# Optimization experiments

Measured on AMD Instinct MI355X. Metric: run time of the kernel, lower is better.

## Reference

```python
import jax, jax.numpy as jnp
import numpy as np

N_NODES = 100000
N_EDGES = 1600000
D_IN, D_HID, D_OUT = 64, 64, 32


def _glorot(key, shape):
    fan_in, fan_out = shape[0], shape[1]
    lim = np.sqrt(6.0 / (fan_in + fan_out)).astype(np.float32)
    return jax.random.uniform(key, shape, jnp.float32, -lim, lim)


def setup_inputs() -> dict:
    key = jax.random.key(0)
    ks = jax.random.split(key, 12)
    x = jax.random.normal(ks[0], (N_NODES, D_IN), jnp.float32)
    edge_index = jax.random.randint(ks[1], (2, N_EDGES), 0, N_NODES, jnp.int64)
    return {
        "x": x,
        "edge_index": edge_index,
        # SAGEConv 1 (in->hid): lin_l (aggregated neighbors, with bias), lin_r (root, no bias)
        "Wl1": _glorot(ks[2], (D_IN, D_HID)),
        "Wr1": _glorot(ks[3], (D_IN, D_HID)),
        "b1": jnp.zeros((D_HID,), jnp.float32),
        # SAGEConv 2 (hid->out)
        "Wl2": _glorot(ks[4], (D_HID, D_OUT)),
        "Wr2": _glorot(ks[5], (D_HID, D_OUT)),
        "b2": jnp.zeros((D_OUT,), jnp.float32),
        # trust head: Linear(32,16) -> ReLU -> Linear(16,1) -> Sigmoid (dropout inert in eval)
        "Wt1": _glorot(ks[6], (D_OUT, 16)),
        "bt1": jnp.zeros((16,), jnp.float32),
        "Wt2": _glorot(ks[7], (16, 1)),
        "bt2": jnp.zeros((1,), jnp.float32),
    }


def _sage_conv(x, src, dst, Wl, Wr, b):
    # mean-aggregate neighbor messages: msg flows src -> dst
    msg = x[src]                                              # [E, d] gather
    agg_sum = jax.ops.segment_sum(msg, dst, num_segments=N_NODES)
    deg = jax.ops.segment_sum(jnp.ones((src.shape[0],), x.dtype), dst,
                              num_segments=N_NODES)
    agg = agg_sum / jnp.maximum(deg, 1.0)[:, None]            # zero-degree -> 0
    return agg @ Wl + x @ Wr + b


def reference(x, edge_index, Wl1, Wr1, b1, Wl2, Wr2, b2, Wt1, bt1, Wt2, bt2):
    src, dst = edge_index[0], edge_index[1]
    h = _sage_conv(x, src, dst, Wl1, Wr1, b1)
    h = jax.nn.relu(h)                    # dropout p=0.3 inert in eval
    h = _sage_conv(h, src, dst, Wl2, Wr2, b2)
    t = jax.nn.relu(h @ Wt1 + bt1)        # dropout p=0.2 inert in eval
    trust = jax.nn.sigmoid(t @ Wt2 + bt2)
    return h, trust
```

## Files before the change

kernel.cpp:

```cpp
#include <hip/hip_runtime.h>
#include <math.h>


#define NBUCK   1563
#define BCAP    1536
#define BKCHUNK 4096

typedef __attribute__((ext_vector_type(8))) __bf16 bf16x8;
typedef __attribute__((ext_vector_type(4))) float  f32x4;

union BU { bf16x8 v; unsigned short u[8]; };

__device__ inline unsigned short f2bf(float x) {
    unsigned u = __float_as_uint(x);
    unsigned r = u + 0x7fffu + ((u >> 16) & 1u);
    return (unsigned short)(r >> 16);
}
__device__ inline unsigned pack2(float a, float b) {
    return (unsigned)f2bf(a) | ((unsigned)f2bf(b) << 16);
}
__device__ inline float bflo(unsigned u) { return __uint_as_float(u << 16); }
__device__ inline float bfhi(unsigned u) { return __uint_as_float(u & 0xffff0000u); }
__device__ inline float bf2f(unsigned short h) { return __uint_as_float((unsigned)h << 16); }

__global__ __launch_bounds__(256) void k_w(
    const float* __restrict__ Wl1, const float* __restrict__ Wr1,
    unsigned short* __restrict__ Wf)
{
    int tid = threadIdx.x;
    for (int idx = tid; idx < 1024; idx += 256) {
        int q = idx >> 6;
        int l = idx & 63;
        int pass = q >> 3, nf = (q >> 1) & 3, kf = q & 1;
        const float* W = pass ? Wr1 : Wl1;
        int col  = nf * 16 + (l & 15);
        int krow = kf * 32 + (l >> 4) * 8;
        unsigned short hi8[8], lo8[8];
        #pragma unroll
        for (int e = 0; e < 8; ++e) {
            float w = W[(krow + e) * 64 + col];
            unsigned short h = f2bf(w);
            hi8[e] = h;
            lo8[e] = f2bf(w - bf2f(h));
        }
        #pragma unroll
        for (int e = 0; e < 8; ++e) {
            Wf[(q * 2 + 0) * 512 + l * 8 + e] = hi8[e];
            Wf[(q * 2 + 1) * 512 + l * 8 + e] = lo8[e];
        }
    }
}

__global__ __launch_bounds__(256) void k_m1(
    const float* __restrict__ x,
    const unsigned short* __restrict__ Wf, const float* __restrict__ b1,
    unsigned* __restrict__ u16b, float* __restrict__ v,
    const int* __restrict__ src, const int* __restrict__ dst,
    int* __restrict__ gcnt, unsigned* __restrict__ pairs,
    int N, int E, int GB, int BKB)
{
    __shared__ int hist[NBUCK];
    int tid = threadIdx.x;
    int g = blockIdx.x / 5, r5 = blockIdx.x % 5;

    if (r5 == 4) {
        if (g >= BKB) return;
        int e0 = g * BKCHUNK;
        int e1 = min(e0 + BKCHUNK, E);

        for (int i = tid; i < NBUCK; i += 256) hist[i] = 0;
        __syncthreads();
        for (int e = e0 + tid; e < e1; e += 256)
            atomicAdd(&hist[((unsigned)dst[e]) >> 6], 1);
        __syncthreads();
        int cnt[7], base[7];
        #pragma unroll
        for (int t = 0; t < 7; ++t) {
            int i = tid + t * 256;
            cnt[t] = (i < NBUCK) ? hist[i] : 0;
        }
        #pragma unroll
        for (int t = 0; t < 7; ++t) {
            int i = tid + t * 256;
            base[t] = (i < NBUCK) ? atomicAdd(&gcnt[i], cnt[t]) : 0;
        }
        #pragma unroll
        for (int t = 0; t < 7; ++t) {
            int i = tid + t * 256;
            if (i < NBUCK) hist[i] = i * BCAP + base[t];
        }
        __syncthreads();
        for (int e = e0 + tid; e < e1; e += 256) {
            int t = dst[e];
            int b = ((unsigned)t) >> 6;
            int pos = atomicAdd(&hist[b], 1);
            if (pos < (b + 1) * BCAP)
                pairs[pos] = (unsigned)src[e] | ((unsigned)(t & 63) << 17);
        }
        return;
    }

    int tile = 4 * g + r5;
    if (tile >= GB) return;
    int nblk = tile * 64;

    int l  = tid & 63, wv = tid >> 6;
    int la = l & 15,   g4 = l >> 4;
    int arow = nblk + wv * 16 + la;
    bool rowOK = (arow < N);

    BU ahi[2], alo[2];
    #pragma unroll
    for (int kf = 0; kf < 2; ++kf) {
        float xv[8];
        if (rowOK) {
            const float* xp = &x[(size_t)arow * 64 + kf * 32 + g4 * 8];
            float4 p0 = *(const float4*)xp;
            float4 p1 = *(const float4*)(xp + 4);
            xv[0] = p0.x; xv[1] = p0.y; xv[2] = p0.z; xv[3] = p0.w;
            xv[4] = p1.x; xv[5] = p1.y; xv[6] = p1.z; xv[7] = p1.w;
        } else {
            #pragma unroll
            for (int e = 0; e < 8; ++e) xv[e] = 0.0f;
        }
        #pragma unroll
        for (int e = 0; e < 8; ++e) {
            unsigned short h = f2bf(xv[e]);
            ahi[kf].u[e] = h;
            alo[kf].u[e] = f2bf(xv[e] - bf2f(h));
        }
    }

    unsigned short* u16 = (unsigned short*)u16b;

    #pragma unroll
    for (int pass = 0; pass < 2; ++pass) {
        #pragma unroll
        for (int nf = 0; nf < 4; ++nf) {
            int n0 = nf * 16;
            f32x4 acc = {0.f, 0.f, 0.f, 0.f};
            #pragma unroll
            for (int kf = 0; kf < 2; ++kf) {
                int q2 = ((pass * 4 + nf) * 2 + kf) * 2;
                bf16x8 bhi = *(const bf16x8*)&Wf[(q2 + 0) * 512 + l * 8];
                bf16x8 blo = *(const bf16x8*)&Wf[(q2 + 1) * 512 + l * 8];
                acc = __builtin_amdgcn_mfma_f32_16x16x32_bf16(ahi[kf].v, bhi, acc, 0, 0, 0);
                acc = __builtin_amdgcn_mfma_f32_16x16x32_bf16(alo[kf].v, bhi, acc, 0, 0, 0);
                acc = __builtin_amdgcn_mfma_f32_16x16x32_bf16(ahi[kf].v, blo, acc, 0, 0, 0);
            }
            if (pass == 0) {
                #pragma unroll
                for (int r = 0; r < 4; ++r) {
                    int nd = nblk + wv * 16 + g4 * 4 + r;
                    if (nd < N)
                        u16[(size_t)nd * 64 + n0 + la] = f2bf(acc[r]);
                }
            } else {
                float bb = b1[n0 + la];
                #pragma unroll
                for (int r = 0; r < 4; ++r) {
                    int nd = nblk + wv * 16 + g4 * 4 + r;
                    if (nd < N)
                        v[(size_t)nd * 64 + n0 + la] = acc[r] + bb;
                }
            }
        }
    }
}

__global__ __launch_bounds__(512) void k_m2(
    const unsigned* __restrict__ pairs, const int* __restrict__ gcnt,
    const unsigned* __restrict__ u16b, const float* __restrict__ v,
    const float* __restrict__ Wl2, const float* __restrict__ Wr2,
    const float* __restrict__ b2,
    unsigned* __restrict__ P16b, float* __restrict__ Qout,
    int2* __restrict__ nodeOff, int* __restrict__ adjG, int N)
{
    __shared__ float sH[64 * 66];
    __shared__ float sW[64 * 64];
    __shared__ int   sAdj[BCAP];
    __shared__ int   sOff[65];
    __shared__ int   sCur[64];
    int tid = threadIdx.x;
    int b = blockIdx.x;
    int nodeBase = b * 64;
    int base = b * BCAP;
    int count = min(gcnt[b], BCAP);
    const unsigned* pp = pairs + (size_t)b * BCAP;

    for (int i = tid * 4; i < 64 * 64; i += 2048) {
        int k = i >> 6, n = i & 63;
        const float* Wsrc = (n < 32) ? (Wl2 + k * 32 + n) : (Wr2 + k * 32 + (n - 32));
        *(float4*)&sW[k * 64 + n] = *(const float4*)Wsrc;
    }
    if (tid < 64) sCur[tid] = 0;
    __syncthreads();

    for (int j = tid; j < count; j += 512)
        atomicAdd(&sCur[(pp[j] >> 17) & 63], 1);
    __syncthreads();
    if (tid < 64) {
        int c = sCur[tid];
        int incl = c;
        #pragma unroll
        for (int off = 1; off < 64; off <<= 1) {
            int t = __shfl_up(incl, off);
            if (tid >= off) incl += t;
        }
        sOff[tid] = incl - c;
        if (tid == 63) sOff[64] = incl;
    }
    __syncthreads();
    if (tid < 64) {
        sCur[tid] = sOff[tid];
        int node = nodeBase + tid;
        if (node < N)
            nodeOff[node] = make_int2(base + sOff[tid], sOff[tid + 1] - sOff[tid]);
    }
    __syncthreads();
    for (int j = tid; j < count; j += 512) {
        unsigned e = pp[j];
        int pos = atomicAdd(&sCur[(e >> 17) & 63], 1);
        sAdj[pos] = (int)(e & 0x1FFFFu);
    }
    __syncthreads();
    for (int j = tid; j < count; j += 512) adjG[base + j] = sAdj[j];

    int hw = tid >> 5, lane = tid & 31;
    for (int r = 0; r < 4; ++r) {
        int nl = hw * 4 + r;
        int node = nodeBase + nl;
        float h0 = 0.0f, h1v = 0.0f;
        if (node < N) {
            int beg = sOff[nl], end = sOff[nl + 1];
            float lo[8] = {0,0,0,0,0,0,0,0}, hi[8] = {0,0,0,0,0,0,0,0};
            int i = beg;
            for (; i + 8 <= end; i += 8) {
                int s[8];
                #pragma unroll
                for (int j = 0; j < 8; ++j) s[j] = sAdj[i + j];
                #pragma unroll
                for (int j = 0; j < 8; ++j) {
                    unsigned w = u16b[(size_t)s[j] * 32 + lane];
                    lo[j] += bflo(w); hi[j] += bfhi(w);
                }
            }
            for (; i < end; ++i) {
                unsigned w = u16b[(size_t)sAdj[i] * 32 + lane];
                lo[0] += bflo(w); hi[0] += bfhi(w);
            }
            float mlo = ((lo[0]+lo[1])+(lo[2]+lo[3])) + ((lo[4]+lo[5])+(lo[6]+lo[7]));
            float mhi = ((hi[0]+hi[1])+(hi[2]+hi[3])) + ((hi[4]+hi[5])+(hi[6]+hi[7]));
            int deg = end - beg;
            float invd = (deg > 0) ? 1.0f / (float)deg : 1.0f;
            float2 vv = ((const float2*)v)[(size_t)node * 32 + lane];
            h0  = fmaxf(mlo * invd + vv.x, 0.0f);
            h1v = fmaxf(mhi * invd + vv.y, 0.0f);
        }
        *(float2*)&sH[nl * 66 + 2 * lane] = make_float2(h0, h1v);
    }
    __syncthreads();

    int ng = tid & 15;
    int mg = tid >> 4;
    int m0 = mg * 2, n0 = ng * 4;

    float acc[2][4];
    #pragma unroll
    for (int mi = 0; mi < 2; ++mi)
        #pragma unroll
        for (int ni = 0; ni < 4; ++ni) acc[mi][ni] = 0.0f;

    #pragma unroll 8
    for (int k = 0; k < 64; ++k) {
        float a0 = sH[(m0 + 0) * 66 + k];
        float a1 = sH[(m0 + 1) * 66 + k];
        float4 w = *(float4*)&sW[k * 64 + n0];
        float wv[4] = {w.x, w.y, w.z, w.w};
        #pragma unroll
        for (int ni = 0; ni < 4; ++ni) {
            acc[0][ni] = fmaf(a0, wv[ni], acc[0][ni]);
            acc[1][ni] = fmaf(a1, wv[ni], acc[1][ni]);
        }
    }

    if (n0 < 32) {
        #pragma unroll
        for (int mi = 0; mi < 2; ++mi) {
            int node = nodeBase + m0 + mi;
            if (node >= N) continue;
            uint2 pk;
            pk.x = pack2(acc[mi][0], acc[mi][1]);
            pk.y = pack2(acc[mi][2], acc[mi][3]);
            *(uint2*)&P16b[(size_t)node * 16 + (n0 >> 1)] = pk;
        }
    } else {
        float4 b0 = *(const float4*)&b2[n0 - 32];
        #pragma unroll
        for (int mi = 0; mi < 2; ++mi) {
            int node = nodeBase + m0 + mi;
            if (node >= N) continue;
            *(float4*)&Qout[(size_t)node * 32 + (n0 - 32)] =
                make_float4(acc[mi][0]+b0.x, acc[mi][1]+b0.y,
                            acc[mi][2]+b0.z, acc[mi][3]+b0.w);
        }
    }
}

__global__ __launch_bounds__(256) void k_a2(
    const int2* __restrict__ nodeOff, const int* __restrict__ adj,
    const unsigned* __restrict__ P16b, const float* __restrict__ Q,
    const float* __restrict__ Wt1, const float* __restrict__ bt1,
    const float* __restrict__ Wt2, const float* __restrict__ bt2,
    float* __restrict__ out_h, float* __restrict__ out_trust, int N)
{
    __shared__ float sWt1[32 * 16];
    __shared__ float sWt2[16];
    for (int i = threadIdx.x; i < 512; i += 256) sWt1[i] = Wt1[i];
    if (threadIdx.x < 16) sWt2[threadIdx.x] = Wt2[threadIdx.x];
    __syncthreads();

    int n = blockIdx.x * 16 + (threadIdx.x >> 4);
    int lane = threadIdx.x & 15;
    if (n >= N) return;

    int2 od = nodeOff[n];
    int beg = od.x, end = od.x + od.y;
    float lo[8] = {0,0,0,0,0,0,0,0}, hi[8] = {0,0,0,0,0,0,0,0};
    int i = beg;
    for (; i + 8 <= end; i += 8) {
        int s[8];
        #pragma unroll
        for (int j = 0; j < 8; ++j) s[j] = adj[i + j];
        #pragma unroll
        for (int j = 0; j < 8; ++j) {
            unsigned w = P16b[(size_t)s[j] * 16 + lane];
            lo[j] += bflo(w); hi[j] += bfhi(w);
        }
    }
    for (; i < end; ++i) {
        unsigned w = P16b[(size_t)adj[i] * 16 + lane];
        lo[0] += bflo(w); hi[0] += bfhi(w);
    }
    float invd = (od.y > 0) ? 1.0f / (float)od.y : 1.0f;
    float mlo = (((lo[0]+lo[1])+(lo[2]+lo[3])) + ((lo[4]+lo[5])+(lo[6]+lo[7]))) * invd;
    float mhi = (((hi[0]+hi[1])+(hi[2]+hi[3])) + ((hi[4]+hi[5])+(hi[6]+hi[7]))) * invd;

    float2 qv = ((const float2*)Q)[(size_t)n * 16 + lane];
    float hx = mlo + qv.x;
    float hy = mhi + qv.y;

    ((float2*)out_h)[(size_t)n * 16 + lane] = make_float2(hx, hy);

    float t = bt1[lane];
    #pragma unroll
    for (int k = 0; k < 16; ++k) {
        float hlo = __shfl(hx, k, 16);
        float hhi = __shfl(hy, k, 16);
        t += hlo * sWt1[(2 * k) * 16 + lane] + hhi * sWt1[(2 * k + 1) * 16 + lane];
    }
    t = fmaxf(t, 0.0f);
    float z = t * sWt2[lane];
    z += __shfl_xor(z, 1);
    z += __shfl_xor(z, 2);
    z += __shfl_xor(z, 4);
    z += __shfl_xor(z, 8);
    if (lane == 0) out_trust[n] = 1.0f / (1.0f + expf(-(z + bt2[0])));
}


extern "C" void kernel_launch(void* const* d_in, const int* in_sizes, int n_in,
                              void* d_out, int out_size, void* d_ws, size_t ws_size,
                              hipStream_t stream)
{
    const float* x   = (const float*)d_in[0];
    const int*   ei  = (const int*)d_in[1];
    const float* Wl1 = (const float*)d_in[2];
    const float* Wr1 = (const float*)d_in[3];
    const float* b1  = (const float*)d_in[4];
    const float* Wl2 = (const float*)d_in[5];
    const float* Wr2 = (const float*)d_in[6];
    const float* b2  = (const float*)d_in[7];
    const float* Wt1 = (const float*)d_in[8];
    const float* bt1 = (const float*)d_in[9];
    const float* Wt2 = (const float*)d_in[10];
    const float* bt2 = (const float*)d_in[11];

    const int N = in_sizes[0] / 64;
    const int E = in_sizes[1] / 2;
    const int* src = ei;
    const int* dst = ei + E;

    unsigned* pairs  = (unsigned*)d_ws;
    unsigned* u16b   = pairs + (size_t)NBUCK * BCAP;
    float*    v      = (float*)(u16b + (size_t)N * 32);
    unsigned* P16b   = (unsigned*)(v + (size_t)N * 64);
    float*    Q      = (float*)(P16b + (size_t)N * 16);
    int2*     nodeOff= (int2*)(Q + (size_t)N * 32);
    int*      adj    = (int*)(nodeOff + N);
    int*      gcnt   = adj + (size_t)NBUCK * BCAP;
    unsigned short* Wf = (unsigned short*)(gcnt + 2048);

    hipMemsetAsync(gcnt, 0, 2048 * sizeof(int), stream);

    k_w<<<1, 256, 0, stream>>>(Wl1, Wr1, Wf);

    const int GB  = (N + 63) / 64;
    const int BKB = (E + BKCHUNK - 1) / BKCHUNK;
    int grp = (GB + 3) / 4 > BKB ? (GB + 3) / 4 : BKB;
    k_m1<<<5 * grp, 256, 0, stream>>>(x, Wf, b1, u16b, v,
                                      src, dst, gcnt, pairs, N, E, GB, BKB);
    k_m2<<<NBUCK, 512, 0, stream>>>(pairs, gcnt, u16b, v, Wl2, Wr2, b2,
                                    P16b, Q, nodeOff, adj, N);

    float* out_h     = (float*)d_out;
    float* out_trust = out_h + (size_t)N * 32;
    k_a2<<<(N + 15) / 16, 256, 0, stream>>>(nodeOff, adj, P16b, Q,
                                            Wt1, bt1, Wt2, bt2,
                                            out_h, out_trust, N);
}
```

Measured before the change: 231.4 us.

## Use split-bf16 MFMA for layer-2 GEMM and enlarge bucketing chunks

Replaces the scalar FP32 FMA GEMM in the second SAGE layer with bf16 MFMA instructions, using a hi/lo split of both activations and weights (three MFMAs per step) to keep close-to-FP32 accuracy. Layer-2 weights are now pre-split by the weight-prep kernel instead of being staged as FP32 in shared memory, which frees shared memory in k_m2. The edge-bucketing blocks in k_m1 now each handle four times as many edges, and the interleave ratio becomes 16 GEMM tiles per bucketing block. This means fewer global atomics on the bucket counters, but each bucketing block does a longer serial pass.

```diff
diff --git a/kernel.cpp b/kernel.cpp
--- a/kernel.cpp
+++ b/kernel.cpp
@@ -4,7 +4,8 @@
 
 #define NBUCK   1563
 #define BCAP    1536
-#define BKCHUNK 4096
+#define BKCHUNK 16384
+#define RT      16
 
 typedef __attribute__((ext_vector_type(8))) __bf16 bf16x8;
 typedef __attribute__((ext_vector_type(4))) float  f32x4;
@@ -22,31 +23,58 @@
 __device__ inline float bflo(unsigned u) { return __uint_as_float(u << 16); }
 __device__ inline float bfhi(unsigned u) { return __uint_as_float(u & 0xffff0000u); }
 __device__ inline float bf2f(unsigned short h) { return __uint_as_float((unsigned)h << 16); }
+__device__ inline unsigned packhl(float x) {
+    unsigned short h = f2bf(x);
+    unsigned short l = f2bf(x - bf2f(h));
+    return (unsigned)h | ((unsigned)l << 16);
+}
 
 __global__ __launch_bounds__(256) void k_w(
     const float* __restrict__ Wl1, const float* __restrict__ Wr1,
+    const float* __restrict__ Wl2, const float* __restrict__ Wr2,
     unsigned short* __restrict__ Wf)
 {
     int tid = threadIdx.x;
-    for (int idx = tid; idx < 1024; idx += 256) {
-        int q = idx >> 6;
-        int l = idx & 63;
-        int pass = q >> 3, nf = (q >> 1) & 3, kf = q & 1;
-        const float* W = pass ? Wr1 : Wl1;
-        int col  = nf * 16 + (l & 15);
-        int krow = kf * 32 + (l >> 4) * 8;
+    for (int idx = tid; idx < 1536; idx += 256) {
         unsigned short hi8[8], lo8[8];
+        int base;
+        if (idx < 1024) {
+            int q = idx >> 6;
+            int l = idx & 63;
+            int pass = q >> 3, nf = (q >> 1) & 3, kf = q & 1;
+            const float* W = pass ? Wr1 : Wl1;
+            int col  = nf * 16 + (l & 15);
+            int krow = kf * 32 + (l >> 4) * 8;
+            #pragma unroll
+            for (int e = 0; e < 8; ++e) {
+                float w = W[(krow + e) * 64 + col];
+                unsigned short h = f2bf(w);
+                hi8[e] = h;
+                lo8[e] = f2bf(w - bf2f(h));
+            }
+            base = (q * 2) * 512 + l * 8;
+        } else {
+            int i2 = idx - 1024;
+            int q2 = i2 >> 6;
+            int l = i2 & 63;
+            int ntile = q2 >> 1, kf = q2 & 1;
+            int col  = ntile * 16 + (l & 15);
+            const float* W = (col < 32) ? Wl2 : Wr2;
+            int c = col & 31;
+            int krow = kf * 32 + (l >> 4) * 8;
+            #pragma unroll
+            for (int e = 0; e < 8; ++e) {
+                float w = W[(krow + e) * 32 + c];
+                unsigned short h = f2bf(w);
+                hi8[e] = h;
+                lo8[e] = f2bf(w - bf2f(h));
+            }
+            base = (32 + q2 * 2) * 512 + l * 8;
+        }
         #pragma unroll
         for (int e = 0; e < 8; ++e) {
-            float w = W[(krow + e) * 64 + col];
-            unsigned short h = f2bf(w);
-            hi8[e] = h;
-            lo8[e] = f2bf(w - bf2f(h));
-        }
-        #pragma unroll
-        for (int e = 0; e < 8; ++e) {
-            Wf[(q * 2 + 0) * 512 + l * 8 + e] = hi8[e];
-            Wf[(q * 2 + 1) * 512 + l * 8 + e] = lo8[e];
+            Wf[base + e]       = hi8[e];
+            Wf[base + 512 + e] = lo8[e];
         }
     }
 }
@@ -61,9 +89,9 @@
 {
     __shared__ int hist[NBUCK];
     int tid = threadIdx.x;
-    int g = blockIdx.x / 5, r5 = blockIdx.x % 5;
-
-    if (r5 == 4) {
+    int g = blockIdx.x / (RT + 1), r = blockIdx.x % (RT + 1);
+
+    if (r == RT) {
         if (g >= BKB) return;
         int e0 = g * BKCHUNK;
         int e1 = min(e0 + BKCHUNK, E);
@@ -100,7 +128,7 @@
         return;
     }
 
-    int tile = 4 * g + r5;
+    int tile = RT * g + r;
     if (tile >= GB) return;
     int nblk = tile * 64;
 
@@ -150,18 +178,18 @@
             }
             if (pass == 0) {
                 #pragma unroll
-                for (int r = 0; r < 4; ++r) {
-                    int nd = nblk + wv * 16 + g4 * 4 + r;
+                for (int rr = 0; rr < 4; ++rr) {
+                    int nd = nblk + wv * 16 + g4 * 4 + rr;
                     if (nd < N)
-                        u16[(size_t)nd * 64 + n0 + la] = f2bf(acc[r]);
+                        u16[(size_t)nd * 64 + n0 + la] = f2bf(acc[rr]);
                 }
             } else {
                 float bb = b1[n0 + la];
                 #pragma unroll
-                for (int r = 0; r < 4; ++r) {
-                    int nd = nblk + wv * 16 + g4 * 4 + r;
+                for (int rr = 0; rr < 4; ++rr) {
+                    int nd = nblk + wv * 16 + g4 * 4 + rr;
                     if (nd < N)
-                        v[(size_t)nd * 64 + n0 + la] = acc[r] + bb;
+                        v[(size_t)nd * 64 + n0 + la] = acc[rr] + bb;
                 }
             }
         }
@@ -171,13 +199,11 @@
 __global__ __launch_bounds__(512) void k_m2(
     const unsigned* __restrict__ pairs, const int* __restrict__ gcnt,
     const unsigned* __restrict__ u16b, const float* __restrict__ v,
-    const float* __restrict__ Wl2, const float* __restrict__ Wr2,
-    const float* __restrict__ b2,
+    const unsigned short* __restrict__ Wf, const float* __restrict__ b2,
     unsigned* __restrict__ P16b, float* __restrict__ Qout,
     int2* __restrict__ nodeOff, int* __restrict__ adjG, int N)
 {
-    __shared__ float sH[64 * 66];
-    __shared__ float sW[64 * 64];
+    __shared__ unsigned sHu[64 * 76];
     __shared__ int   sAdj[BCAP];
     __shared__ int   sOff[65];
     __shared__ int   sCur[64];
@@ -188,11 +214,6 @@
     int count = min(gcnt[b], BCAP);
     const unsigned* pp = pairs + (size_t)b * BCAP;
 
-    for (int i = tid * 4; i < 64 * 64; i += 2048) {
-        int k = i >> 6, n = i & 63;
-        const float* Wsrc = (n < 32) ? (Wl2 + k * 32 + n) : (Wr2 + k * 32 + (n - 32));
-        *(float4*)&sW[k * 64 + n] = *(const float4*)Wsrc;
-    }
     if (tid < 64) sCur[tid] = 0;
     __syncthreads();
 
@@ -257,52 +278,58 @@
             h0  = fmaxf(mlo * invd + vv.x, 0.0f);
             h1v = fmaxf(mhi * invd + vv.y, 0.0f);
         }
-        *(float2*)&sH[nl * 66 + 2 * lane] = make_float2(h0, h1v);
-    }
-    __syncthreads();
-
-    int ng = tid & 15;
-    int mg = tid >> 4;
-    int m0 = mg * 2, n0 = ng * 4;
-
-    float acc[2][4];
+        *(uint2*)&sHu[nl * 76 + 2 * lane] = make_uint2(packhl(h0), packhl(h1v));
+    }
+    __syncthreads();
+
+    int w = tid >> 6, l = tid & 63;
+    int la = l & 15, g4 = l >> 4;
+    int mtile = w & 3, nt2 = (w >> 2) * 2;
+
+    BU ahi[2], alo[2];
     #pragma unroll
-    for (int mi = 0; mi < 2; ++mi)
-        #pragma unroll
-        for (int ni = 0; ni < 4; ++ni) acc[mi][ni] = 0.0f;
-
-    #pragma unroll 8
-    for (int k = 0; k < 64; ++k) {
-        float a0 = sH[(m0 + 0) * 66 + k];
-        float a1 = sH[(m0 + 1) * 66 + k];
-        float4 w = *(float4*)&sW[k * 64 + n0];
-        float wv[4] = {w.x, w.y, w.z, w.w};
-        #pragma unroll
-        for (int ni = 0; ni < 4; ++ni) {
-            acc[0][ni] = fmaf(a0, wv[ni], acc[0][ni]);
-            acc[1][ni] = fmaf(a1, wv[ni], acc[1][ni]);
-        }
-    }
-
-    if (n0 < 32) {
-        #pragma unroll
-        for (int mi = 0; mi < 2; ++mi) {
-            int node = nodeBase + m0 + mi;
-            if (node >= N) continue;
-            uint2 pk;
-            pk.x = pack2(acc[mi][0], acc[mi][1]);
-            pk.y = pack2(acc[mi][2], acc[mi][3]);
-            *(uint2*)&P16b[(size_t)node * 16 + (n0 >> 1)] = pk;
-        }
-    } else {
-        float4 b0 = *(const float4*)&b2[n0 - 32];
-        #pragma unroll
-        for (int mi = 0; mi < 2; ++mi) {
-            int node = nodeBase + m0 + mi;
-            if (node >= N) continue;
-            *(float4*)&Qout[(size_t)node * 32 + (n0 - 32)] =
-                make_float4(acc[mi][0]+b0.x, acc[mi][1]+b0.y,
-                            acc[mi][2]+b0.z, acc[mi][3]+b0.w);
+    for (int kf = 0; kf < 2; ++kf) {
+        const unsigned* hp = &sHu[(mtile * 16 + la) * 76 + kf * 32 + g4 * 8];
+        uint4 a0 = *(const uint4*)hp;
+        uint4 a1 = *(const uint4*)(hp + 4);
+        unsigned wv8[8] = {a0.x, a0.y, a0.z, a0.w, a1.x, a1.y, a1.z, a1.w};
+        #pragma unroll
+        for (int e = 0; e < 8; ++e) {
+            ahi[kf].u[e] = (unsigned short)wv8[e];
+            alo[kf].u[e] = (unsigned short)(wv8[e] >> 16);
+        }
+    }
+
+    unsigned short* Pus = (unsigned short*)P16b;
+    #pragma unroll
+    for (int j = 0; j < 2; ++j) {
+        int ntile = nt2 + j;
+        f32x4 acc = {0.f, 0.f, 0.f, 0.f};
+        #pragma unroll
+        for (int kf = 0; kf < 2; ++kf) {
+            const unsigned short* Wq = Wf + (size_t)(32 + (ntile * 2 + kf) * 2) * 512;
+            bf16x8 bhi = *(const bf16x8*)&Wq[l * 8];
+            bf16x8 blo = *(const bf16x8*)&Wq[512 + l * 8];
+            acc = __builtin_amdgcn_mfma_f32_16x16x32_bf16(ahi[kf].v, bhi, acc, 0, 0, 0);
+            acc = __builtin_amdgcn_mfma_f32_16x16x32_bf16(alo[kf].v, bhi, acc, 0, 0, 0);
+            acc = __builtin_amdgcn_mfma_f32_16x16x32_bf16(ahi[kf].v, blo, acc, 0, 0, 0);
+        }
+        int col = ntile * 16 + la;
+        if (col < 32) {
+            #pragma unroll
+            for (int rr = 0; rr < 4; ++rr) {
+                int node = nodeBase + mtile * 16 + g4 * 4 + rr;
+                if (node < N)
+                    Pus[(size_t)node * 32 + col] = f2bf(acc[rr]);
+            }
+        } else {
+            float bb = b2[col - 32];
+            #pragma unroll
+            for (int rr = 0; rr < 4; ++rr) {
+                int node = nodeBase + mtile * 16 + g4 * 4 + rr;
+                if (node < N)
+                    Qout[(size_t)node * 32 + (col - 32)] = acc[rr] + bb;
+            }
         }
     }
 }
@@ -403,14 +430,14 @@
 
     hipMemsetAsync(gcnt, 0, 2048 * sizeof(int), stream);
 
-    k_w<<<1, 256, 0, stream>>>(Wl1, Wr1, Wf);
+    k_w<<<1, 256, 0, stream>>>(Wl1, Wr1, Wl2, Wr2, Wf);
 
     const int GB  = (N + 63) / 64;
     const int BKB = (E + BKCHUNK - 1) / BKCHUNK;
-    int grp = (GB + 3) / 4 > BKB ? (GB + 3) / 4 : BKB;
-    k_m1<<<5 * grp, 256, 0, stream>>>(x, Wf, b1, u16b, v,
-                                      src, dst, gcnt, pairs, N, E, GB, BKB);
-    k_m2<<<NBUCK, 512, 0, stream>>>(pairs, gcnt, u16b, v, Wl2, Wr2, b2,
+    int grp = (GB + RT - 1) / RT > BKB ? (GB + RT - 1) / RT : BKB;
+    k_m1<<<(RT + 1) * grp, 256, 0, stream>>>(x, Wf, b1, u16b, v,
+                                             src, dst, gcnt, pairs, N, E, GB, BKB);
+    k_m2<<<NBUCK, 512, 0, stream>>>(pairs, gcnt, u16b, v, Wf, b2,
                                     P16b, Q, nodeOff, adj, N);
 
     float* out_h     = (float*)d_out;
```

New measurement: 249.9 us. +8.0%, slower.
